# Kernel optimization log

Measured on AMD Instinct MI355X. Metric: run time of the kernel, lower is better.

Reference implementation:

```python
import jax, jax.numpy as jnp
import numpy as np

D = 384      # ViT-S feature dim (feat_dim_lookup['s'])
H = 6        # module forces num_heads = 6
L = 12       # ViT-S depth
RATIO = 0.1  # attention_mask_ratio
EPS = 1e-6


def layernorm(x, g, b):
    m = x.mean(-1, keepdims=True)
    v = ((x - m) ** 2).mean(-1, keepdims=True)
    return (x - m) * jax.lax.rsqrt(v + EPS) * g + b


def masked_attn(x, w_qkv, b_qkv, w_o, b_o):
    # Patch._fix_attn_masking: full softmax attention, threshold at ratio*row_max, renormalize.
    B, N, Dm = x.shape
    dh = Dm // H
    qkv = (x @ w_qkv + b_qkv).reshape(B, N, 3, H, dh)
    q = qkv[:, :, 0].transpose(0, 2, 1, 3)  # [B,H,N,dh]
    k = qkv[:, :, 1].transpose(0, 2, 1, 3)
    v = qkv[:, :, 2].transpose(0, 2, 1, 3)
    scores = jnp.einsum('bhqd,bhkd->bhqk', q, k) * (dh ** -0.5)
    attn = jax.nn.softmax(scores, axis=-1)
    thresh = RATIO * attn.max(axis=-1, keepdims=True)
    attn = jnp.where(attn >= thresh, attn, 0.0)
    attn = attn / attn.sum(axis=-1, keepdims=True)  # re-normalize
    out = jnp.einsum('bhqk,bhkd->bhqd', attn, v)
    out = out.transpose(0, 2, 1, 3).reshape(B, N, Dm)
    return out @ w_o + b_o, attn


def block(x, p):
    w_qkv, b_qkv, w_o, b_o, g1, be1, g2, be2, w1, b1, w2, b2 = p
    h, attn = masked_attn(layernorm(x, g1, be1), w_qkv, b_qkv, w_o, b_o)
    x = x + h
    h = layernorm(x, g2, be2) @ w1 + b1
    h = jax.nn.gelu(h, approximate=False) @ w2 + b2
    return x + h, attn


def setup_inputs() -> dict:
    key = jax.random.key(0)
    ks = jax.random.split(key, 8)
    B, N = 2, 962  # 2 transforms; (1+(160-8)//5)**2 + 1 cls = 962 tokens
    s = 0.02
    return {
        'x': jax.random.normal(ks[0], (B, N, D), jnp.float32),
        'w_qkv': jax.random.normal(ks[1], (L, D, 3 * D), jnp.float32) * s,
        'b_qkv': jnp.zeros((L, 3 * D), jnp.float32),
        'w_proj': jax.random.normal(ks[2], (L, D, D), jnp.float32) * s,
        'b_proj': jnp.zeros((L, D), jnp.float32),
        'ln1_g': jnp.ones((L, D), jnp.float32),
        'ln1_b': jnp.zeros((L, D), jnp.float32),
        'ln2_g': jnp.ones((L, D), jnp.float32),
        'ln2_b': jnp.zeros((L, D), jnp.float32),
        'w_fc1': jax.random.normal(ks[3], (L, D, 4 * D), jnp.float32) * s,
        'b_fc1': jnp.zeros((L, 4 * D), jnp.float32),
        'w_fc2': jax.random.normal(ks[4], (L, 4 * D, D), jnp.float32) * s,
        'b_fc2': jnp.zeros((L, D), jnp.float32),
        'lnf_g': jnp.ones((D,), jnp.float32),
        'lnf_b': jnp.zeros((D,), jnp.float32),
    }


def reference(x, w_qkv, b_qkv, w_proj, b_proj, ln1_g, ln1_b, ln2_g, ln2_b,
              w_fc1, b_fc1, w_fc2, b_fc2, lnf_g, lnf_b):
    params = (w_qkv, b_qkv, w_proj, b_proj, ln1_g, ln1_b, ln2_g, ln2_b,
              w_fc1, b_fc1, w_fc2, b_fc2)
    first = jax.tree_util.tree_map(lambda a: a[:-1], params)
    last = jax.tree_util.tree_map(lambda a: a[-1], params)

    def scan_fn(h, p):
        h, _ = block(h, p)
        return h, None

    x, _ = jax.lax.scan(scan_fn, x, first)  # blocks 0..L-2
    x, attn = block(x, last)                # last block, keep masked attention
    feats = layernorm(x, lnf_g, lnf_b)      # [B, N, D]
    return feats, attn
```

## Files before the change

kernel.cpp:

```cpp
#include <hip/hip_runtime.h>
#include <hip/hip_bf16.h>
#include <math.h>

typedef __bf16 bf16_t;
typedef __bf16 bf16x8 __attribute__((ext_vector_type(8)));
typedef float f32x4 __attribute__((ext_vector_type(4)));

#define NEGBIG -3.0e38f

typedef __attribute__((address_space(3))) unsigned int lds_u32;
typedef const __attribute__((address_space(1))) unsigned int glb_u32;
static __device__ __forceinline__ void gld16(const void* g, void* l) {
    __builtin_amdgcn_global_load_lds((glb_u32*)g, (lds_u32*)l, 16, 0, 0);
}

__global__ void __launch_bounds__(256) tr_k(
    const float* __restrict__ W, bf16_t* __restrict__ Wt, int K, int N)
{
    __shared__ float T[32][33];
    const size_t per = (size_t)K * N;
    const float* Wl = W + blockIdx.z * per;
    bf16_t* Wtl = Wt + blockIdx.z * per;
    int n0 = blockIdx.x * 32, k0 = blockIdx.y * 32;
    int tx = threadIdx.x & 31, ty = threadIdx.x >> 5;
#pragma unroll
    for (int i = 0; i < 4; ++i)
        T[ty + 8 * i][tx] = Wl[(size_t)(k0 + ty + 8 * i) * N + n0 + tx];
    __syncthreads();
#pragma unroll
    for (int i = 0; i < 4; ++i)
        Wtl[(size_t)(n0 + ty + 8 * i) * K + k0 + tx] = (bf16_t)T[tx][ty + 8 * i];
}

template <int MODE>
__global__ void __launch_bounds__(256) gemm_k(
    const bf16_t* __restrict__ A, const bf16_t* __restrict__ Bt,
    const float* __restrict__ bias, int M, int N, int K,
    bf16_t* __restrict__ outb,
    bf16_t* __restrict__ qb, bf16_t* __restrict__ kb, bf16_t* __restrict__ vtb)
{
    __shared__ alignas(16) bf16_t As[2][4096];
    __shared__ alignas(16) bf16_t Bs[2][4096];

    const int tid  = threadIdx.x;
    const int wave = tid >> 6, lane = tid & 63;
    const int m0 = blockIdx.y * 64, n0 = blockIdx.x * 64;
    const int rb = (wave >> 1) * 32, cb = (wave & 1) * 32;
    const int q4 = lane >> 4, mm = lane & 15;

    const int r8 = lane >> 3;
    const int cs = ((lane & 7) ^ r8) * 8;
    const int w2 = wave * 2;
    const bf16_t* gA0 = A  + (size_t)(m0 + w2 * 8 + r8)       * K + cs;
    const bf16_t* gA1 = A  + (size_t)(m0 + (w2 + 1) * 8 + r8) * K + cs;
    const bf16_t* gB0 = Bt + (size_t)(n0 + w2 * 8 + r8)       * K + cs;
    const bf16_t* gB1 = Bt + (size_t)(n0 + (w2 + 1) * 8 + r8) * K + cs;

    auto stage = [&](int buf, int k0) {
        gld16(gA0 + k0, &As[buf][w2 * 512]);
        gld16(gA1 + k0, &As[buf][(w2 + 1) * 512]);
        gld16(gB0 + k0, &Bs[buf][w2 * 512]);
        gld16(gB1 + k0, &Bs[buf][(w2 + 1) * 512]);
    };

    stage(0, 0);
    f32x4 acc[2][2] = {};
    int cur = 0;
    for (int k0 = 0; k0 < K; k0 += 64) {
        __syncthreads();
        const bool has_next = (k0 + 64 < K);
        if (has_next) stage(cur ^ 1, k0 + 64);
#pragma unroll
        for (int kc = 0; kc < 64; kc += 32) {
            const int sc = (((kc >> 3) + q4) ^ (mm & 7)) * 8;
            bf16x8 a0 = *(const bf16x8*)(&As[cur][(rb + mm) * 64 + sc]);
            bf16x8 a1 = *(const bf16x8*)(&As[cur][(rb + 16 + mm) * 64 + sc]);
            bf16x8 b0 = *(const bf16x8*)(&Bs[cur][(cb + mm) * 64 + sc]);
            bf16x8 b1 = *(const bf16x8*)(&Bs[cur][(cb + 16 + mm) * 64 + sc]);
            acc[0][0] = __builtin_amdgcn_mfma_f32_16x16x32_bf16(a0, b0, acc[0][0], 0, 0, 0);
            acc[0][1] = __builtin_amdgcn_mfma_f32_16x16x32_bf16(a0, b1, acc[0][1], 0, 0, 0);
            acc[1][0] = __builtin_amdgcn_mfma_f32_16x16x32_bf16(a1, b0, acc[1][0], 0, 0, 0);
            acc[1][1] = __builtin_amdgcn_mfma_f32_16x16x32_bf16(a1, b1, acc[1][1], 0, 0, 0);
        }
        if (has_next) cur ^= 1;
    }

#pragma unroll
    for (int i = 0; i < 2; ++i)
#pragma unroll
    for (int j = 0; j < 2; ++j) {
        int gc = n0 + cb + j * 16 + mm;
        float bv = bias[gc];
#pragma unroll
        for (int r = 0; r < 4; ++r) {
            int gr = m0 + rb + i * 16 + q4 * 4 + r;
            if (gr >= M) continue;
            float val = acc[i][j][r] + bv;
            if (MODE == 2) {
                float g = 0.5f * val * (1.0f + erff(val * 0.70710678118654752f));
                outb[(size_t)gr * N + gc] = (bf16_t)g;
            } else {
                int which = gc / 384, rem = gc % 384;
                int h = rem >> 6, d = rem & 63;
                int b = gr / 962, n = gr % 962;
                int bh = b * 6 + h;
                bf16_t bvv = (bf16_t)val;
                if (which == 0)      qb[((size_t)bh * 962 + n) * 64 + d] = bvv;
                else if (which == 1) kb[((size_t)bh * 962 + n) * 64 + d] = bvv;
                else                 vtb[((size_t)bh * 64 + d) * 992 + n] = bvv;
            }
        }
    }
}

template <int KLEN>
__global__ void __launch_bounds__(256) gemm_sp(
    const bf16_t* __restrict__ A, int lda,
    const bf16_t* __restrict__ Bt, int ldb,
    const float* __restrict__ bias, int M, int N,
    float* __restrict__ resid)
{
    __shared__ alignas(16) bf16_t As[2][4096];
    __shared__ alignas(16) bf16_t Bs[2][4096];

    const int tid  = threadIdx.x;
    const int wave = tid >> 6, lane = tid & 63;
    const int m0 = blockIdx.y * 64, n0 = blockIdx.x * 64;
    const int rb = (wave >> 1) * 32, cb = (wave & 1) * 32;
    const int q4 = lane >> 4, mm = lane & 15;
    const int ks = blockIdx.z * KLEN;

    const int r8 = lane >> 3;
    const int cs = ((lane & 7) ^ r8) * 8;
    const int w2 = wave * 2;
    const bf16_t* gA0 = A  + (size_t)(m0 + w2 * 8 + r8)       * lda + ks + cs;
    const bf16_t* gA1 = A  + (size_t)(m0 + (w2 + 1) * 8 + r8) * lda + ks + cs;
    const bf16_t* gB0 = Bt + (size_t)(n0 + w2 * 8 + r8)       * ldb + ks + cs;
    const bf16_t* gB1 = Bt + (size_t)(n0 + (w2 + 1) * 8 + r8) * ldb + ks + cs;

    auto stage = [&](int buf, int k0) {
        gld16(gA0 + k0, &As[buf][w2 * 512]);
        gld16(gA1 + k0, &As[buf][(w2 + 1) * 512]);
        gld16(gB0 + k0, &Bs[buf][w2 * 512]);
        gld16(gB1 + k0, &Bs[buf][(w2 + 1) * 512]);
    };

    stage(0, 0);
    f32x4 acc[2][2] = {};
    int cur = 0;
    for (int k0 = 0; k0 < KLEN; k0 += 64) {
        __syncthreads();
        const bool has_next = (k0 + 64 < KLEN);
        if (has_next) stage(cur ^ 1, k0 + 64);
#pragma unroll
        for (int kc = 0; kc < 64; kc += 32) {
            const int sc = (((kc >> 3) + q4) ^ (mm & 7)) * 8;
            bf16x8 a0 = *(const bf16x8*)(&As[cur][(rb + mm) * 64 + sc]);
            bf16x8 a1 = *(const bf16x8*)(&As[cur][(rb + 16 + mm) * 64 + sc]);
            bf16x8 b0 = *(const bf16x8*)(&Bs[cur][(cb + mm) * 64 + sc]);
            bf16x8 b1 = *(const bf16x8*)(&Bs[cur][(cb + 16 + mm) * 64 + sc]);
            acc[0][0] = __builtin_amdgcn_mfma_f32_16x16x32_bf16(a0, b0, acc[0][0], 0, 0, 0);
            acc[0][1] = __builtin_amdgcn_mfma_f32_16x16x32_bf16(a0, b1, acc[0][1], 0, 0, 0);
            acc[1][0] = __builtin_amdgcn_mfma_f32_16x16x32_bf16(a1, b0, acc[1][0], 0, 0, 0);
            acc[1][1] = __builtin_amdgcn_mfma_f32_16x16x32_bf16(a1, b1, acc[1][1], 0, 0, 0);
        }
        if (has_next) cur ^= 1;
    }

#pragma unroll
    for (int i = 0; i < 2; ++i)
#pragma unroll
    for (int j = 0; j < 2; ++j) {
        int gc = n0 + cb + j * 16 + mm;
        float bv = (blockIdx.z == 0) ? bias[gc] : 0.f;
#pragma unroll
        for (int r = 0; r < 4; ++r) {
            int gr = m0 + rb + i * 16 + q4 * 4 + r;
            if (gr >= M) continue;
            atomicAdd(&resid[(size_t)gr * N + gc], acc[i][j][r] + bv);
        }
    }
}

__global__ void __launch_bounds__(256) attn_k(
    const bf16_t* __restrict__ qb, const bf16_t* __restrict__ kb,
    const bf16_t* __restrict__ vtb, bf16_t* __restrict__ attnout,
    float* __restrict__ attn_save)
{
    __shared__ alignas(16) bf16_t S[16][1000];

    const int tid  = threadIdx.x;
    const int wave = tid >> 6, lane = tid & 63;
    const int q4 = lane >> 4, mm = lane & 15;
    const int bh = blockIdx.y, qt = blockIdx.x;
    const int qrow0 = qt * 16;

    int qr = qrow0 + mm; if (qr > 961) qr = 961;
    const bf16_t* qptr = qb + ((size_t)bh * 962 + qr) * 64 + q4 * 8;
    bf16x8 aq0 = *(const bf16x8*)(qptr);
    bf16x8 aq1 = *(const bf16x8*)(qptr + 32);

    for (int ct = wave; ct < 61; ct += 4) {
        int kr = ct * 16 + mm; if (kr > 961) kr = 961;
        const bf16_t* kptr = kb + ((size_t)bh * 962 + kr) * 64 + q4 * 8;
        bf16x8 b0 = *(const bf16x8*)(kptr);
        bf16x8 b1 = *(const bf16x8*)(kptr + 32);
        f32x4 acc = {};
        acc = __builtin_amdgcn_mfma_f32_16x16x32_bf16(aq0, b0, acc, 0, 0, 0);
        acc = __builtin_amdgcn_mfma_f32_16x16x32_bf16(aq1, b1, acc, 0, 0, 0);
        int col = ct * 16 + mm;
#pragma unroll
        for (int r = 0; r < 4; ++r) {
            int row = q4 * 4 + r;
            if (col < 962) S[row][col] = (bf16_t)(acc[r] * 0.125f);
        }
    }
    for (int idx = tid; idx < 16 * 38; idx += 256) {
        int r = idx / 38, c = 962 + idx % 38;
        S[r][c] = (bf16_t)NEGBIG;
    }
    __syncthreads();

    const int trow = tid >> 4, ti = tid & 15;
    float e[8][8];
    float mx = NEGBIG;
#pragma unroll
    for (int t = 0; t < 8; ++t) {
        int c8 = ti * 8 + 128 * t;
        bf16x8 xv;
        if (c8 < 1000) xv = *(const bf16x8*)(&S[trow][c8]);
        else {
#pragma unroll
            for (int j = 0; j < 8; ++j) xv[j] = (bf16_t)NEGBIG;
        }
#pragma unroll
        for (int j = 0; j < 8; ++j) { e[t][j] = (float)xv[j]; mx = fmaxf(mx, e[t][j]); }
    }
#pragma unroll
    for (int off = 8; off > 0; off >>= 1) mx = fmaxf(mx, __shfl_xor(mx, off, 16));

    float sum = 0.f;
#pragma unroll
    for (int t = 0; t < 8; ++t)
#pragma unroll
    for (int j = 0; j < 8; ++j) {
        float ev = __expf(e[t][j] - mx);
        e[t][j] = ev;
        if (ev >= 0.1f) sum += ev;
    }
#pragma unroll
    for (int off = 8; off > 0; off >>= 1) sum += __shfl_xor(sum, off, 16);
    float inv = 1.0f / sum;

    int row_g = qrow0 + trow;
#pragma unroll
    for (int t = 0; t < 8; ++t) {
        int c8 = ti * 8 + 128 * t;
        if (c8 >= 1000) continue;
        bf16x8 pv;
#pragma unroll
        for (int j = 0; j < 8; ++j) {
            float pp = (e[t][j] >= 0.1f) ? e[t][j] * inv : 0.f;
            e[t][j] = pp;
            pv[j] = (bf16_t)pp;
        }
        *(bf16x8*)(&S[trow][c8]) = pv;
        if (attn_save && row_g < 962) {
#pragma unroll
            for (int j = 0; j < 8; ++j)
                if (c8 + j < 962)
                    attn_save[((size_t)bh * 962 + row_g) * 962 + c8 + j] = e[t][j];
        }
    }
    __syncthreads();

    const int wc0 = wave * 16;
    f32x4 o = {};
    for (int kc = 0; kc < 31; ++kc) {
        bf16x8 pa = *(const bf16x8*)(&S[mm][kc * 32 + q4 * 8]);
        bf16x8 vb = *(const bf16x8*)(vtb + ((size_t)bh * 64 + wc0 + mm) * 992 + kc * 32 + q4 * 8);
        o = __builtin_amdgcn_mfma_f32_16x16x32_bf16(pa, vb, o, 0, 0, 0);
    }
    int b = bh / 6, h = bh % 6;
#pragma unroll
    for (int r = 0; r < 4; ++r) {
        int qrr = qrow0 + q4 * 4 + r;
        if (qrr < 962)
            attnout[((size_t)(b * 962 + qrr)) * 384 + h * 64 + wc0 + mm] = (bf16_t)o[r];
    }
}

template <typename OT>
__global__ void __launch_bounds__(256) ln_k(
    const float* __restrict__ x, const float* __restrict__ g,
    const float* __restrict__ b, OT* __restrict__ out)
{
    int t = blockIdx.x * 4 + (threadIdx.x >> 6);
    int lane = threadIdx.x & 63;
    const float* xp = x + (size_t)t * 384;
    float v[6];
    float s = 0.f;
#pragma unroll
    for (int i = 0; i < 6; ++i) { v[i] = xp[lane + 64 * i]; s += v[i]; }
    for (int off = 32; off > 0; off >>= 1) s += __shfl_xor(s, off);
    float mean = s * (1.0f / 384.0f);
    float s2 = 0.f;
#pragma unroll
    for (int i = 0; i < 6; ++i) { float d = v[i] - mean; s2 += d * d; }
    for (int off = 32; off > 0; off >>= 1) s2 += __shfl_xor(s2, off);
    float rstd = rsqrtf(s2 * (1.0f / 384.0f) + 1e-6f);
#pragma unroll
    for (int i = 0; i < 6; ++i) {
        int c = lane + 64 * i;
        float y = (v[i] - mean) * rstd * g[c] + b[c];
        out[(size_t)t * 384 + c] = (OT)y;
    }
}

extern "C" void kernel_launch(void* const* d_in, const int* in_sizes, int n_in,
                              void* d_out, int out_size, void* d_ws, size_t ws_size,
                              hipStream_t stream)
{
    const float* xin    = (const float*)d_in[0];
    const float* w_qkv  = (const float*)d_in[1];
    const float* b_qkv  = (const float*)d_in[2];
    const float* w_proj = (const float*)d_in[3];
    const float* b_proj = (const float*)d_in[4];
    const float* ln1g   = (const float*)d_in[5];
    const float* ln1b   = (const float*)d_in[6];
    const float* ln2g   = (const float*)d_in[7];
    const float* ln2b   = (const float*)d_in[8];
    const float* w_fc1  = (const float*)d_in[9];
    const float* b_fc1  = (const float*)d_in[10];
    const float* w_fc2  = (const float*)d_in[11];
    const float* b_fc2  = (const float*)d_in[12];
    const float* lnfg   = (const float*)d_in[13];
    const float* lnfb   = (const float*)d_in[14];

    float* feats     = (float*)d_out;
    float* attn_save = feats + 738816;

    char* p = (char*)d_ws;
    auto alloc = [&](size_t bytes) {
        char* r = p;
        p += (bytes + 255) & ~(size_t)255;
        return r;
    };
    float*  x_f32   = (float*)alloc(1924ull * 384 * 4);
    bf16_t* xn      = (bf16_t*)alloc(1984ull * 384 * 2);
    bf16_t* qbuf    = (bf16_t*)alloc(12ull * 962 * 64 * 2);
    bf16_t* kbuf    = (bf16_t*)alloc(12ull * 962 * 64 * 2);
    bf16_t* vtbuf   = (bf16_t*)alloc(12ull * 64 * 992 * 2);
    bf16_t* attnout = (bf16_t*)alloc(1984ull * 384 * 2);
    bf16_t* mlp1    = (bf16_t*)alloc(1984ull * 1536 * 2);
    bf16_t* wt_qkv  = (bf16_t*)alloc(12ull * 1152 * 384 * 2);
    bf16_t* wt_proj = (bf16_t*)alloc(12ull * 384 * 384 * 2);
    bf16_t* wt_fc1  = (bf16_t*)alloc(12ull * 1536 * 384 * 2);
    bf16_t* wt_fc2  = (bf16_t*)alloc(12ull * 384 * 1536 * 2);

    tr_k<<<dim3(36, 12, 12), dim3(256), 0, stream>>>(w_qkv,  wt_qkv,  384, 1152);
    tr_k<<<dim3(12, 12, 12), dim3(256), 0, stream>>>(w_proj, wt_proj, 384, 384);
    tr_k<<<dim3(48, 12, 12), dim3(256), 0, stream>>>(w_fc1,  wt_fc1,  384, 1536);
    tr_k<<<dim3(12, 48, 12), dim3(256), 0, stream>>>(w_fc2,  wt_fc2,  1536, 384);

    hipMemcpyAsync(x_f32, xin, 738816ull * 4, hipMemcpyDeviceToDevice, stream);

    for (int l = 0; l < 12; ++l) {
        ln_k<bf16_t><<<dim3(481), dim3(256), 0, stream>>>(x_f32, ln1g + l * 384, ln1b + l * 384, xn);
        gemm_k<0><<<dim3(18, 31), dim3(256), 0, stream>>>(
            xn, wt_qkv + (size_t)l * 1152 * 384, b_qkv + l * 1152,
            1924, 1152, 384, nullptr, qbuf, kbuf, vtbuf);
        attn_k<<<dim3(61, 12), dim3(256), 0, stream>>>(
            qbuf, kbuf, vtbuf, attnout, (l == 11) ? attn_save : (float*)nullptr);
        gemm_sp<192><<<dim3(6, 31, 2), dim3(256), 0, stream>>>(
            attnout, 384, wt_proj + (size_t)l * 384 * 384, 384, b_proj + l * 384,
            1924, 384, x_f32);
        ln_k<bf16_t><<<dim3(481), dim3(256), 0, stream>>>(x_f32, ln2g + l * 384, ln2b + l * 384, xn);
        gemm_k<2><<<dim3(24, 31), dim3(256), 0, stream>>>(
            xn, wt_fc1 + (size_t)l * 1536 * 384, b_fc1 + l * 1536,
            1924, 1536, 384, mlp1, nullptr, nullptr, nullptr);
        gemm_sp<384><<<dim3(6, 31, 4), dim3(256), 0, stream>>>(
            mlp1, 1536, wt_fc2 + (size_t)l * 384 * 1536, 1536, b_fc2 + l * 384,
            1924, 384, x_f32);
    }
    ln_k<float><<<dim3(481), dim3(256), 0, stream>>>(x_f32, lnfg, lnfb, feats);
}
```

Before: 1.074 ms.

## Fuse LayerNorm into QKV and FC1 GEMMs and merge weight transposes

Removes the separate LayerNorm kernels before the QKV and FC1 GEMMs. Each GEMM block now loads its 64x384 fp32 rows, computes the normalization, and keeps the whole normalized A tile in LDS. Only B is double-buffered, with a 32-wide K step. The four weight-transpose launches are also merged into one kernel. The costs are that LayerNorm is recomputed by every column block, LDS use grows to about 48KB per block, and variance now uses a single-pass formula on bf16-rounded inputs, which may slightly change numerics.

```diff
diff --git a/kernel.cpp b/kernel.cpp
--- a/kernel.cpp
+++ b/kernel.cpp
@@ -14,14 +14,25 @@
     __builtin_amdgcn_global_load_lds((glb_u32*)g, (lds_u32*)l, 16, 0, 0);
 }
 
-__global__ void __launch_bounds__(256) tr_k(
-    const float* __restrict__ W, bf16_t* __restrict__ Wt, int K, int N)
+__global__ void __launch_bounds__(256) tr_all(
+    const float* __restrict__ w0, bf16_t* __restrict__ t0,
+    const float* __restrict__ w1, bf16_t* __restrict__ t1,
+    const float* __restrict__ w2, bf16_t* __restrict__ t2,
+    const float* __restrict__ w3, bf16_t* __restrict__ t3)
 {
     __shared__ float T[32][33];
-    const size_t per = (size_t)K * N;
-    const float* Wl = W + blockIdx.z * per;
-    bf16_t* Wtl = Wt + blockIdx.z * per;
-    int n0 = blockIdx.x * 32, k0 = blockIdx.y * 32;
+    int id = blockIdx.x;
+    const float* W; bf16_t* Wt; int K, N, nx;
+    if (id < 5184)       { W = w0; Wt = t0; K = 384;  N = 1152; nx = 36; }
+    else if (id < 6912)  { id -= 5184;  W = w1; Wt = t1; K = 384;  N = 384;  nx = 12; }
+    else if (id < 13824) { id -= 6912;  W = w2; Wt = t2; K = 384;  N = 1536; nx = 48; }
+    else                 { id -= 13824; W = w3; Wt = t3; K = 1536; N = 384;  nx = 12; }
+    const int per = nx * (K >> 5);
+    const int z = id / per, rem = id % per;
+    const int n0 = (rem % nx) * 32, k0 = (rem / nx) * 32;
+    const size_t base = (size_t)z * K * N;
+    const float* Wl = W + base;
+    bf16_t* Wtl = Wt + base;
     int tx = threadIdx.x & 31, ty = threadIdx.x >> 5;
 #pragma unroll
     for (int i = 0; i < 4; ++i)
@@ -33,14 +44,15 @@
 }
 
 template <int MODE>
-__global__ void __launch_bounds__(256) gemm_k(
-    const bf16_t* __restrict__ A, const bf16_t* __restrict__ Bt,
-    const float* __restrict__ bias, int M, int N, int K,
-    bf16_t* __restrict__ outb,
+__global__ void __launch_bounds__(256) gemm_fln(
+    const float* __restrict__ X, const bf16_t* __restrict__ Bt,
+    const float* __restrict__ bias,
+    const float* __restrict__ lg, const float* __restrict__ lb,
+    int M, int N, bf16_t* __restrict__ outb,
     bf16_t* __restrict__ qb, bf16_t* __restrict__ kb, bf16_t* __restrict__ vtb)
 {
-    __shared__ alignas(16) bf16_t As[2][4096];
-    __shared__ alignas(16) bf16_t Bs[2][4096];
+    __shared__ alignas(16) bf16_t An[64 * 384];
+    __shared__ alignas(16) bf16_t Bs[2][64 * 32];
 
     const int tid  = threadIdx.x;
     const int wave = tid >> 6, lane = tid & 63;
@@ -48,40 +60,75 @@
     const int rb = (wave >> 1) * 32, cb = (wave & 1) * 32;
     const int q4 = lane >> 4, mm = lane & 15;
 
-    const int r8 = lane >> 3;
-    const int cs = ((lane & 7) ^ r8) * 8;
-    const int w2 = wave * 2;
-    const bf16_t* gA0 = A  + (size_t)(m0 + w2 * 8 + r8)       * K + cs;
-    const bf16_t* gA1 = A  + (size_t)(m0 + (w2 + 1) * 8 + r8) * K + cs;
-    const bf16_t* gB0 = Bt + (size_t)(n0 + w2 * 8 + r8)       * K + cs;
-    const bf16_t* gB1 = Bt + (size_t)(n0 + (w2 + 1) * 8 + r8) * K + cs;
-
-    auto stage = [&](int buf, int k0) {
-        gld16(gA0 + k0, &As[buf][w2 * 512]);
-        gld16(gA1 + k0, &As[buf][(w2 + 1) * 512]);
-        gld16(gB0 + k0, &Bs[buf][w2 * 512]);
-        gld16(gB1 + k0, &Bs[buf][(w2 + 1) * 512]);
+    const int brow = wave * 16 + (lane >> 2);
+    const int bsw  = ((lane & 3) ^ ((lane >> 2) & 3)) * 8;
+    const bf16_t* gB = Bt + (size_t)(n0 + brow) * 384 + bsw;
+    auto stageB = [&](int buf, int k0) {
+        gld16(gB + k0, &Bs[buf][wave * 512]);
     };
-
-    stage(0, 0);
+    stageB(0, 0);
+
+    {
+        const int trow = tid >> 2, ti = tid & 3;
+        const bool valid = (m0 + trow) < M;
+        const float* xr = X + (size_t)(m0 + trow) * 384 + ti * 96;
+        bf16x8 areg[12];
+        float s = 0.f, s2 = 0.f;
+#pragma unroll
+        for (int j = 0; j < 12; ++j) {
+            float4 f0 = make_float4(0.f, 0.f, 0.f, 0.f), f1 = f0;
+            if (valid) {
+                f0 = *(const float4*)(xr + j * 8);
+                f1 = *(const float4*)(xr + j * 8 + 4);
+            }
+            bf16x8 v = { (bf16_t)f0.x, (bf16_t)f0.y, (bf16_t)f0.z, (bf16_t)f0.w,
+                         (bf16_t)f1.x, (bf16_t)f1.y, (bf16_t)f1.z, (bf16_t)f1.w };
+            areg[j] = v;
+#pragma unroll
+            for (int e = 0; e < 8; ++e) { float f = (float)v[e]; s += f; s2 += f * f; }
+        }
+        s  += __shfl_xor(s, 1, 4);  s  += __shfl_xor(s, 2, 4);
+        s2 += __shfl_xor(s2, 1, 4); s2 += __shfl_xor(s2, 2, 4);
+        float mean = s * (1.0f / 384.0f);
+        float var  = s2 * (1.0f / 384.0f) - mean * mean;
+        float rstd = rsqrtf(fmaxf(var, 0.f) + 1e-6f);
+#pragma unroll
+        for (int j = 0; j < 12; ++j) {
+            int gcol = ti * 96 + j * 8;
+            float4 g0 = *(const float4*)(lg + gcol);
+            float4 g1 = *(const float4*)(lg + gcol + 4);
+            float4 b0 = *(const float4*)(lb + gcol);
+            float4 b1 = *(const float4*)(lb + gcol + 4);
+            float gg[8] = { g0.x, g0.y, g0.z, g0.w, g1.x, g1.y, g1.z, g1.w };
+            float bb[8] = { b0.x, b0.y, b0.z, b0.w, b1.x, b1.y, b1.z, b1.w };
+            bf16x8 o;
+#pragma unroll
+            for (int e = 0; e < 8; ++e)
+                o[e] = (bf16_t)(((float)areg[j][e] - mean) * rstd * gg[e] + bb[e]);
+            int slot = ((gcol >> 3) & 7) ^ (trow & 7);
+            *(bf16x8*)(&An[trow * 384 + (gcol & ~63) + slot * 8]) = o;
+        }
+    }
+    __syncthreads();
+
     f32x4 acc[2][2] = {};
     int cur = 0;
-    for (int k0 = 0; k0 < K; k0 += 64) {
-        __syncthreads();
-        const bool has_next = (k0 + 64 < K);
-        if (has_next) stage(cur ^ 1, k0 + 64);
-#pragma unroll
-        for (int kc = 0; kc < 64; kc += 32) {
-            const int sc = (((kc >> 3) + q4) ^ (mm & 7)) * 8;
-            bf16x8 a0 = *(const bf16x8*)(&As[cur][(rb + mm) * 64 + sc]);
-            bf16x8 a1 = *(const bf16x8*)(&As[cur][(rb + 16 + mm) * 64 + sc]);
-            bf16x8 b0 = *(const bf16x8*)(&Bs[cur][(cb + mm) * 64 + sc]);
-            bf16x8 b1 = *(const bf16x8*)(&Bs[cur][(cb + 16 + mm) * 64 + sc]);
-            acc[0][0] = __builtin_amdgcn_mfma_f32_16x16x32_bf16(a0, b0, acc[0][0], 0, 0, 0);
-            acc[0][1] = __builtin_amdgcn_mfma_f32_16x16x32_bf16(a0, b1, acc[0][1], 0, 0, 0);
-            acc[1][0] = __builtin_amdgcn_mfma_f32_16x16x32_bf16(a1, b0, acc[1][0], 0, 0, 0);
-            acc[1][1] = __builtin_amdgcn_mfma_f32_16x16x32_bf16(a1, b1, acc[1][1], 0, 0, 0);
-        }
+    for (int k0 = 0; k0 < 384; k0 += 32) {
+        if (k0) __syncthreads();
+        const bool has_next = (k0 + 32 < 384);
+        if (has_next) stageB(cur ^ 1, k0 + 32);
+        const int gcA = ((k0 & 32) >> 3) + q4;
+        const int kbA = k0 & ~63;
+        const int rA0 = rb + mm, rA1 = rb + 16 + mm;
+        bf16x8 a0 = *(const bf16x8*)(&An[rA0 * 384 + kbA + ((gcA ^ (rA0 & 7)) * 8)]);
+        bf16x8 a1 = *(const bf16x8*)(&An[rA1 * 384 + kbA + ((gcA ^ (rA1 & 7)) * 8)]);
+        const int rB0 = cb + mm, rB1 = cb + 16 + mm;
+        bf16x8 b0 = *(const bf16x8*)(&Bs[cur][rB0 * 32 + ((q4 ^ (rB0 & 3)) * 8)]);
+        bf16x8 b1 = *(const bf16x8*)(&Bs[cur][rB1 * 32 + ((q4 ^ (rB1 & 3)) * 8)]);
+        acc[0][0] = __builtin_amdgcn_mfma_f32_16x16x32_bf16(a0, b0, acc[0][0], 0, 0, 0);
+        acc[0][1] = __builtin_amdgcn_mfma_f32_16x16x32_bf16(a0, b1, acc[0][1], 0, 0, 0);
+        acc[1][0] = __builtin_amdgcn_mfma_f32_16x16x32_bf16(a1, b0, acc[1][0], 0, 0, 0);
+        acc[1][1] = __builtin_amdgcn_mfma_f32_16x16x32_bf16(a1, b1, acc[1][1], 0, 0, 0);
         if (has_next) cur ^= 1;
     }
 
@@ -290,10 +337,9 @@
     }
 }
 
-template <typename OT>
 __global__ void __launch_bounds__(256) ln_k(
     const float* __restrict__ x, const float* __restrict__ g,
-    const float* __restrict__ b, OT* __restrict__ out)
+    const float* __restrict__ b, float* __restrict__ out)
 {
     int t = blockIdx.x * 4 + (threadIdx.x >> 6);
     int lane = threadIdx.x & 63;
@@ -312,8 +358,7 @@
 #pragma unroll
     for (int i = 0; i < 6; ++i) {
         int c = lane + 64 * i;
-        float y = (v[i] - mean) * rstd * g[c] + b[c];
-        out[(size_t)t * 384 + c] = (OT)y;
+        out[(size_t)t * 384 + c] = (v[i] - mean) * rstd * g[c] + b[c];
     }
 }
 
@@ -347,7 +392,6 @@
         return r;
     };
     float*  x_f32   = (float*)alloc(1924ull * 384 * 4);
-    bf16_t* xn      = (bf16_t*)alloc(1984ull * 384 * 2);
     bf16_t* qbuf    = (bf16_t*)alloc(12ull * 962 * 64 * 2);
     bf16_t* kbuf    = (bf16_t*)alloc(12ull * 962 * 64 * 2);
     bf16_t* vtbuf   = (bf16_t*)alloc(12ull * 64 * 992 * 2);
@@ -358,30 +402,28 @@
     bf16_t* wt_fc1  = (bf16_t*)alloc(12ull * 1536 * 384 * 2);
     bf16_t* wt_fc2  = (bf16_t*)alloc(12ull * 384 * 1536 * 2);
 
-    tr_k<<<dim3(36, 12, 12), dim3(256), 0, stream>>>(w_qkv,  wt_qkv,  384, 1152);
-    tr_k<<<dim3(12, 12, 12), dim3(256), 0, stream>>>(w_proj, wt_proj, 384, 384);
-    tr_k<<<dim3(48, 12, 12), dim3(256), 0, stream>>>(w_fc1,  wt_fc1,  384, 1536);
-    tr_k<<<dim3(12, 48, 12), dim3(256), 0, stream>>>(w_fc2,  wt_fc2,  1536, 384);
+    tr_all<<<dim3(20736), dim3(256), 0, stream>>>(
+        w_qkv, wt_qkv, w_proj, wt_proj, w_fc1, wt_fc1, w_fc2, wt_fc2);
 
     hipMemcpyAsync(x_f32, xin, 738816ull * 4, hipMemcpyDeviceToDevice, stream);
 
     for (int l = 0; l < 12; ++l) {
-        ln_k<bf16_t><<<dim3(481), dim3(256), 0, stream>>>(x_f32, ln1g + l * 384, ln1b + l * 384, xn);
-        gemm_k<0><<<dim3(18, 31), dim3(256), 0, stream>>>(
-            xn, wt_qkv + (size_t)l * 1152 * 384, b_qkv + l * 1152,
-            1924, 1152, 384, nullptr, qbuf, kbuf, vtbuf);
+        gemm_fln<0><<<dim3(18, 31), dim3(256), 0, stream>>>(
+            x_f32, wt_qkv + (size_t)l * 1152 * 384, b_qkv + l * 1152,
+            ln1g + l * 384, ln1b + l * 384,
+            1924, 1152, nullptr, qbuf, kbuf, vtbuf);
         attn_k<<<dim3(61, 12), dim3(256), 0, stream>>>(
             qbuf, kbuf, vtbuf, attnout, (l == 11) ? attn_save : (float*)nullptr);
         gemm_sp<192><<<dim3(6, 31, 2), dim3(256), 0, stream>>>(
             attnout, 384, wt_proj + (size_t)l * 384 * 384, 384, b_proj + l * 384,
             1924, 384, x_f32);
-        ln_k<bf16_t><<<dim3(481), dim3(256), 0, stream>>>(x_f32, ln2g + l * 384, ln2b + l * 384, xn);
-        gemm_k<2><<<dim3(24, 31), dim3(256), 0, stream>>>(
-            xn, wt_fc1 + (size_t)l * 1536 * 384, b_fc1 + l * 1536,
-            1924, 1536, 384, mlp1, nullptr, nullptr, nullptr);
+        gemm_fln<2><<<dim3(24, 31), dim3(256), 0, stream>>>(
+            x_f32, wt_fc1 + (size_t)l * 1536 * 384, b_fc1 + l * 1536,
+            ln2g + l * 384, ln2b + l * 384,
+            1924, 1536, mlp1, nullptr, nullptr, nullptr);
         gemm_sp<384><<<dim3(6, 31, 4), dim3(256), 0, stream>>>(
             mlp1, 1536, wt_fc2 + (size_t)l * 384 * 1536, 1536, b_fc2 + l * 384,
             1924, 384, x_f32);
     }
-    ln_k<float><<<dim3(481), dim3(256), 0, stream>>>(x_f32, lnfg, lnfb, feats);
-}
+    ln_k<<<dim3(481), dim3(256), 0, stream>>>(x_f32, lnfg, lnfb, feats);
+}
```

New measurement: 1.776 ms. 65.4% more time.
